# Kernel optimization log

Hardware: AMD Instinct MI355X
Metric: run time of the kernel (lower is better)

Reference implementation:

```python
import jax, jax.numpy as jnp
import numpy as np

KP_EXTENT = 1.2  # influence radius of each kernel point (init arg KP_extent)
SHADOW_COORD = 1e6  # shadow point coordinate for padding (as in original KPConv)


def setup_inputs() -> dict:
    key = jax.random.key(0)
    k1, k2, k3, k4, k5, k6 = jax.random.split(key, 6)
    N, Ns, H, K, Cin, Cout = 20000, 20000, 40, 15, 128, 128
    q_pts = jax.random.uniform(k1, (N, 3), dtype=jnp.float32)
    s_pts = jax.random.uniform(k2, (Ns, 3), dtype=jnp.float32)
    neighb_inds = jax.random.randint(k3, (N, H), 0, Ns, dtype=jnp.int32)
    x = jax.random.normal(k4, (Ns, Cin), dtype=jnp.float32)
    # kernel point positions inside the sphere (stand-in for load_kernels output)
    kernel_points = jax.random.normal(k5, (K, 3), dtype=jnp.float32) * 0.5
    kernel_points = kernel_points.at[0].set(0.0)  # fixed='center'
    weights = jax.random.normal(k6, (K, Cin, Cout), dtype=jnp.float32) * (1.0 / np.sqrt(Cin))
    return {"q_pts": q_pts, "s_pts": s_pts, "neighb_inds": neighb_inds,
            "x": x, "kernel_points": kernel_points, "weights": weights}


def reference(q_pts, s_pts, neighb_inds, x, kernel_points, weights):
    # Pad support points with a far-away shadow point and features with a zero row,
    # so out-of-range neighbor index Ns contributes nothing (original KPConv trick).
    s_pad = jnp.concatenate([s_pts, jnp.full((1, s_pts.shape[1]), SHADOW_COORD, s_pts.dtype)], axis=0)
    x_pad = jnp.concatenate([x, jnp.zeros((1, x.shape[1]), x.dtype)], axis=0)

    # Gather neighbor coords, center on query points: [N, H, 3]
    neighbors = s_pad[neighb_inds] - q_pts[:, None, :]

    # Squared distance to every kernel point: [N, H, K]
    diff = neighbors[:, :, None, :] - kernel_points[None, None, :, :]
    sq_dist = jnp.sum(diff * diff, axis=-1)

    # Linear influence weights, aggregation_mode='sum': [N, K, H]
    all_weights = jnp.clip(1.0 - jnp.sqrt(sq_dist) / KP_EXTENT, 0.0, None)
    all_weights = jnp.swapaxes(all_weights, 1, 2)

    # Gather neighbor features: [N, H, Cin]
    neighb_x = x_pad[neighb_inds]

    # Influence-weighted aggregation over neighbors: [N, K, Cin]
    weighted = jnp.einsum('nkh,nhc->nkc', all_weights, neighb_x)

    # Per-kernel-point linear maps, summed over kernel points: [N, Cout]
    out = jnp.einsum('nkc,kcd->nd', weighted, weights)
    return out
```

## Files before the change

kernel.cpp:

```cpp
#include <hip/hip_runtime.h>

#define KP   15
#define HN   40
#define CIN  128
#define COUT 128
#define KDIM (KP*CIN)
#define KP_EXT_INV (1.0f/1.2f)

typedef __bf16 bf16x8 __attribute__((ext_vector_type(8)));
typedef float  f32x4  __attribute__((ext_vector_type(4)));

__device__ inline void async_copy16(const void* g, void* lds) {
    __builtin_amdgcn_global_load_lds(
        (const __attribute__((address_space(1))) unsigned int*)g,
        (__attribute__((address_space(3))) unsigned int*)lds, 16, 0, 0);
}

__global__ __launch_bounds__(256)
void kpconv_prep(const float* __restrict__ x, const float* __restrict__ W,
                 __bf16* __restrict__ xb, __bf16* __restrict__ Wt,
                 int nx_elems, int nxB)
{
    __shared__ float sW[32][133];
    const int b = blockIdx.x;
    const int t = threadIdx.x;

    if (b < nxB) {
        const int e0 = (b*256 + t) * 8;
        if (e0 + 8 <= nx_elems) {
            const float4 f0 = *(const float4*)(x + e0);
            const float4 f1 = *(const float4*)(x + e0 + 4);
            bf16x8 v;
            v[0]=(__bf16)f0.x; v[1]=(__bf16)f0.y; v[2]=(__bf16)f0.z; v[3]=(__bf16)f0.w;
            v[4]=(__bf16)f1.x; v[5]=(__bf16)f1.y; v[6]=(__bf16)f1.z; v[7]=(__bf16)f1.w;
            *(bf16x8*)(xb + e0) = v;
        } else {
            for (int e = e0; e < nx_elems; ++e) xb[e] = (__bf16)x[e];
        }
    } else {
        const int kc0 = (b - nxB) * 32;
        #pragma unroll
        for (int i = 0; i < 4; ++i) {
            const int off = t*4 + i*1024;
            const int r = off >> 7, c = off & 127;
            const float4 f = *(const float4*)(W + (size_t)(kc0 + r)*COUT + c);
            sW[r][c+0]=f.x; sW[r][c+1]=f.y; sW[r][c+2]=f.z; sW[r][c+3]=f.w;
        }
        __syncthreads();
        #pragma unroll
        for (int i = 0; i < 2; ++i) {
            const int id = t + i*256;
            const int d  = id >> 2, ch = id & 3;
            bf16x8 v;
            #pragma unroll
            for (int j = 0; j < 8; ++j) v[j] = (__bf16)sW[ch*8 + j][d];
            *(bf16x8*)(Wt + (size_t)d*KDIM + kc0 + ch*8) = v;
        }
    }
}

__global__ __launch_bounds__(256, 4)
void kpconv_aggregate(const float* __restrict__ q_pts,
                      const float* __restrict__ s_pts,
                      const int*   __restrict__ nb,
                      const __bf16* __restrict__ xb,
                      const float* __restrict__ kpts,
                      __bf16* __restrict__ wsA,
                      int N, int Ns)
{
    __shared__ __align__(16) __bf16 sXt[4][4][128][8];
    __shared__ __align__(16) float4 s_nd[4][HN];
    __shared__ int                  s_idx[4][HN];

    const int t  = threadIdx.x;
    const int wv = t >> 6;
    const int l  = t & 63;
    const int n  = blockIdx.x * 4 + wv;

    if (l < HN) {
        int idx = nb[n*HN + l];
        float dx, dy, dz;
        if (idx >= 0 && idx < Ns) {
            dx = s_pts[idx*3+0] - q_pts[n*3+0];
            dy = s_pts[idx*3+1] - q_pts[n*3+1];
            dz = s_pts[idx*3+2] - q_pts[n*3+2];
        } else { idx = 0; dx = dy = dz = 2.0e6f; }
        s_idx[wv][l] = idx;
        s_nd[wv][l]  = make_float4(dx, dy, dz, 0.f);
    }
    __syncthreads();

    const int m = l & 15;
    const int q = l >> 4;
    float kx = 0.f, ky = 0.f, kz = 0.f;
    if (m < KP) { kx = kpts[m*3+0]; ky = kpts[m*3+1]; kz = kpts[m*3+2]; }

    bf16x8 wfrag[2];
    #pragma unroll
    for (int ks = 0; ks < 2; ++ks) {
        #pragma unroll
        for (int j = 0; j < 8; ++j) {
            const int h = ks*32 + q*8 + j;
            float w = 0.f;
            if (m < KP && h < HN) {
                float4 nd = s_nd[wv][h];
                float dx = nd.x - kx, dy = nd.y - ky, dz = nd.z - kz;
                w = fmaxf(1.0f - sqrtf(dx*dx + dy*dy + dz*dz) * KP_EXT_INV, 0.f);
            }
            wfrag[ks][j] = (__bf16)w;
        }
    }

    f32x4 acc[8];
    #pragma unroll
    for (int nt = 0; nt < 8; ++nt) acc[nt] = (f32x4){0.f, 0.f, 0.f, 0.f};

    const int c8 = l & 15;

    for (int ks = 0; ks < 2; ++ks) {
        const int hpBeg = ks ? 16 : 0;
        const int hpEnd = ks ? 20 : 16;
        for (int hp = hpBeg + (l >> 4); hp < hpEnd; hp += 4) {
            const int h0 = 2*hp;
            const uint4 a = *(const uint4*)(xb + (size_t)s_idx[wv][h0  ]*CIN + c8*8);
            const uint4 bb= *(const uint4*)(xb + (size_t)s_idx[wv][h0+1]*CIN + c8*8);
            const unsigned int av[4] = {a.x, a.y, a.z, a.w};
            const unsigned int bv[4] = {bb.x, bb.y, bb.z, bb.w};
            const int hl = h0 - ks*32;
            const int hc = hl >> 3;
            const int dw = hp & 3;
            unsigned int* plane = (unsigned int*)&sXt[wv][hc][0][0];
            #pragma unroll
            for (int j = 0; j < 8; ++j) {
                const unsigned int lo = (av[j>>1] >> ((j&1)*16)) & 0xFFFFu;
                const unsigned int hi = (bv[j>>1] >> ((j&1)*16)) & 0xFFFFu;
                const int p = c8*8 + (j ^ (c8 & 7));
                plane[p*4 + dw] = lo | (hi << 16);
            }
        }
        __syncthreads();

        #pragma unroll
        for (int nt = 0; nt < 8; ++nt) {
            const int cc = nt*16 + m;
            const int p  = (cc & ~7) | ((cc & 7) ^ ((cc >> 3) & 7));
            bf16x8 bfrag = *(const bf16x8*)&sXt[wv][q][p][0];
            acc[nt] = __builtin_amdgcn_mfma_f32_16x16x32_bf16(
                          wfrag[ks], bfrag, acc[nt], 0, 0, 0);
        }
        __syncthreads();
    }

    #pragma unroll
    for (int nt = 0; nt < 8; ++nt) {
        #pragma unroll
        for (int r = 0; r < 4; ++r) {
            const int row = q*4 + r;
            if (row < KP)
                wsA[(size_t)n*KDIM + row*CIN + nt*16 + m] = (__bf16)acc[nt][r];
        }
    }
}

#define BM 32
#define BK 128

__global__ __launch_bounds__(256, 2)
void kpconv_gemm(const __bf16* __restrict__ A,
                 const __bf16* __restrict__ Bt,
                 float* __restrict__ out, int M)
{
    __shared__ __align__(16) __bf16 sA[BM*BK];
    __shared__ __align__(16) __bf16 sB[COUT*BK];

    const int t     = threadIdx.x;
    const int wv    = t >> 6;
    const int l     = t & 63;
    const int mlane = l & 15;
    const int q     = l >> 4;
    const int m0    = blockIdx.x * BM;

    const int rA = t >> 4;
    const int pA = t & 15;

    f32x4 acc[2][2];
    #pragma unroll
    for (int i = 0; i < 2; ++i)
        #pragma unroll
        for (int j = 0; j < 2; ++j) acc[i][j] = (f32x4){0.f,0.f,0.f,0.f};

    for (int k0 = 0; k0 < KDIM; k0 += BK) {
        #pragma unroll
        for (int pass = 0; pass < 2; ++pass) {
            const int r  = rA + pass*16;
            const int ch = pA ^ (r & 15);
            async_copy16(A + (size_t)(m0 + r)*KDIM + k0 + ch*8,
                         (char*)sA + pass*4096 + wv*1024 + l*16);
        }
        #pragma unroll
        for (int pass = 0; pass < 8; ++pass) {
            const int r  = rA + pass*16;
            const int ch = pA ^ (r & 15);
            async_copy16(Bt + (size_t)r*KDIM + k0 + ch*8,
                         (char*)sB + pass*4096 + wv*1024 + l*16);
        }
        __syncthreads();

        #pragma unroll
        for (int ksi = 0; ksi < 4; ++ksi) {
            bf16x8 af[2], bfr[2];
            #pragma unroll
            for (int mt = 0; mt < 2; ++mt) {
                const int row = mt*16 + mlane;
                const int p   = (ksi*4 + q) ^ (row & 15);
                af[mt] = *(const bf16x8*)&sA[row*BK + p*8];
            }
            #pragma unroll
            for (int j = 0; j < 2; ++j) {
                const int row = (wv*2 + j)*16 + mlane;
                const int p   = (ksi*4 + q) ^ (row & 15);
                bfr[j] = *(const bf16x8*)&sB[row*BK + p*8];
            }
            #pragma unroll
            for (int mt = 0; mt < 2; ++mt)
                #pragma unroll
                for (int j = 0; j < 2; ++j)
                    acc[mt][j] = __builtin_amdgcn_mfma_f32_16x16x32_bf16(
                                     af[mt], bfr[j], acc[mt][j], 0, 0, 0);
        }
        __syncthreads();
    }

    #pragma unroll
    for (int mt = 0; mt < 2; ++mt)
        #pragma unroll
        for (int j = 0; j < 2; ++j)
            #pragma unroll
            for (int r = 0; r < 4; ++r)
                out[(size_t)(m0 + mt*16 + q*4 + r)*COUT + (wv*2+j)*16 + mlane]
                    = acc[mt][j][r];
}

#define TM 8
#define WSTR (KP*CIN + 4)

__global__ __launch_bounds__(256, 2)
void kpconv_fused(const float* __restrict__ q_pts,
                  const float* __restrict__ s_pts,
                  const int*   __restrict__ nb,
                  const float* __restrict__ x,
                  const float* __restrict__ kpts,
                  const float* __restrict__ W,
                  float* __restrict__ out,
                  int N, int Ns)
{
    __shared__ float s_kp[KP*3];
    __shared__ float s_nd2[HN*3];
    __shared__ int   s_idx2[HN];
    __shared__ float s_w[KP][HN];
    __shared__ float s_wt[TM*WSTR];

    const int t  = threadIdx.x;
    const int n0 = (int)blockIdx.x * TM;
    if (t < KP*3) s_kp[t] = kpts[t];
    const int c = t & (CIN-1);
    const int g = t >> 7;

    for (int m = 0; m < TM; ++m) {
        const int n = n0 + m;
        if (t < HN) {
            float dx = 1e6f, dy = 1e6f, dz = 1e6f;
            int idx = 0;
            if (n < N) {
                idx = nb[n*HN + t];
                if (idx >= 0 && idx < Ns) {
                    dx = s_pts[idx*3+0] - q_pts[n*3+0];
                    dy = s_pts[idx*3+1] - q_pts[n*3+1];
                    dz = s_pts[idx*3+2] - q_pts[n*3+2];
                } else idx = 0;
            }
            s_idx2[t] = idx;
            s_nd2[t*3+0] = dx; s_nd2[t*3+1] = dy; s_nd2[t*3+2] = dz;
        }
        __syncthreads();
        for (int task = t; task < KP*HN; task += 256) {
            const int k = task / HN;
            const int h = task - k*HN;
            const float dx = s_nd2[h*3+0] - s_kp[k*3+0];
            const float dy = s_nd2[h*3+1] - s_kp[k*3+1];
            const float dz = s_nd2[h*3+2] - s_kp[k*3+2];
            s_w[k][h] = fmaxf(1.0f - sqrtf(dx*dx+dy*dy+dz*dz)*KP_EXT_INV, 0.0f);
        }
        __syncthreads();
        float facc[8];
        #pragma unroll
        for (int j = 0; j < 8; ++j) facc[j] = 0.0f;
        #pragma unroll 8
        for (int h = 0; h < HN; ++h) {
            const float xv = x[s_idx2[h]*CIN + c];
            #pragma unroll
            for (int j = 0; j < 8; ++j) {
                const int k = g + 2*j;
                if (k < KP) facc[j] += s_w[k][h] * xv;
            }
        }
        #pragma unroll
        for (int j = 0; j < 8; ++j) {
            const int k = g + 2*j;
            if (k < KP) s_wt[m*WSTR + k*CIN + c] = facc[j];
        }
        __syncthreads();
    }

    const int m3 = t >> 5;
    const int d0 = (t & 31) * 4;
    const float* wm = &s_wt[m3*WSTR];
    float ax = 0.f, ay = 0.f, az = 0.f, aw = 0.f;
    #pragma unroll 4
    for (int kc = 0; kc < KP*CIN; ++kc) {
        const float  wvv = wm[kc];
        const float4 wr = *(const float4*)&W[kc*COUT + d0];
        ax += wvv * wr.x; ay += wvv * wr.y; az += wvv * wr.z; aw += wvv * wr.w;
    }
    const int n = n0 + m3;
    if (n < N) {
        float4 o; o.x = ax; o.y = ay; o.z = az; o.w = aw;
        *(float4*)&out[n*COUT + d0] = o;
    }
}

extern "C" void kernel_launch(void* const* d_in, const int* in_sizes, int n_in,
                              void* d_out, int out_size, void* d_ws, size_t ws_size,
                              hipStream_t stream) {
    const float* q_pts = (const float*)d_in[0];
    const float* s_pts = (const float*)d_in[1];
    const int*   nb    = (const int*)  d_in[2];
    const float* x     = (const float*)d_in[3];
    const float* kpts  = (const float*)d_in[4];
    const float* W     = (const float*)d_in[5];
    float* out = (float*)d_out;

    const int N  = in_sizes[0] / 3;
    const int Ns = in_sizes[1] / 3;
    const int nx = in_sizes[3];

    const size_t needA = (size_t)N * KDIM * sizeof(__bf16);
    const size_t needB = (size_t)COUT * KDIM * sizeof(__bf16);
    const size_t needX = (size_t)nx * sizeof(__bf16);

    if (ws_size >= needA + needB + needX && (N % 4) == 0 && (N % BM) == 0
        && (KDIM % 32) == 0) {
        __bf16* wsA = (__bf16*)d_ws;
        __bf16* wsB = (__bf16*)((char*)d_ws + needA);
        __bf16* wsX = (__bf16*)((char*)d_ws + needA + needB);

        const int nxB = (nx/8 + 255) / 256;
        const int nwB = KDIM / 32;
        hipLaunchKernelGGL(kpconv_prep, dim3(nxB + nwB), dim3(256), 0, stream,
                           x, W, wsX, wsB, nx, nxB);
        hipLaunchKernelGGL(kpconv_aggregate, dim3(N/4), dim3(256), 0, stream,
                           q_pts, s_pts, nb, wsX, kpts, wsA, N, Ns);
        hipLaunchKernelGGL(kpconv_gemm, dim3(N/BM), dim3(256), 0, stream,
                           wsA, wsB, out, N);
    } else {
        const int grid = (N + TM - 1) / TM;
        hipLaunchKernelGGL(kpconv_fused, dim3(grid), dim3(256), 0, stream,
                           q_pts, s_pts, nb, x, kpts, W, out, N, Ns);
    }
}
```

Baseline: 146.1 us.

## Fuse neighbor aggregation and weight GEMM into one kernel via LDS

Replaces the separate aggregate and GEMM kernels with a single kernel in which each 512-thread block aggregates 16 points into a swizzled LDS tile and then multiplies it against the bf16 weight matrix read directly from global memory with register double-buffering. This removes the round trip of the N x 1920 bf16 intermediate through global memory and one kernel launch. It also uses v_perm for packing and replaces block barriers with lgkmcnt waits inside each wave. In exchange, occupancy drops to one large block per CU with heavy LDS use, and every block re-reads the full weight matrix from cache.

```diff
diff --git a/kernel.cpp b/kernel.cpp
--- a/kernel.cpp
+++ b/kernel.cpp
@@ -6,15 +6,12 @@
 #define COUT 128
 #define KDIM (KP*CIN)
 #define KP_EXT_INV (1.0f/1.2f)
+#define MB   16
+#define NW   8
 
 typedef __bf16 bf16x8 __attribute__((ext_vector_type(8)));
+typedef __bf16 bf16x4 __attribute__((ext_vector_type(4)));
 typedef float  f32x4  __attribute__((ext_vector_type(4)));
-
-__device__ inline void async_copy16(const void* g, void* lds) {
-    __builtin_amdgcn_global_load_lds(
-        (const __attribute__((address_space(1))) unsigned int*)g,
-        (__attribute__((address_space(3))) unsigned int*)lds, 16, 0, 0);
-}
 
 __global__ __launch_bounds__(256)
 void kpconv_prep(const float* __restrict__ x, const float* __restrict__ W,
@@ -59,186 +56,153 @@
     }
 }
 
-__global__ __launch_bounds__(256, 4)
-void kpconv_aggregate(const float* __restrict__ q_pts,
-                      const float* __restrict__ s_pts,
-                      const int*   __restrict__ nb,
-                      const __bf16* __restrict__ xb,
-                      const float* __restrict__ kpts,
-                      __bf16* __restrict__ wsA,
-                      int N, int Ns)
+__global__ __launch_bounds__(512, 1)
+void kpconv_main(const float* __restrict__ q_pts,
+                 const float* __restrict__ s_pts,
+                 const int*   __restrict__ nb,
+                 const __bf16* __restrict__ xb,
+                 const float* __restrict__ kpts,
+                 const __bf16* __restrict__ Wt,
+                 float* __restrict__ out, int N, int Ns)
 {
-    __shared__ __align__(16) __bf16 sXt[4][4][128][8];
-    __shared__ __align__(16) float4 s_nd[4][HN];
-    __shared__ int                  s_idx[4][HN];
+    __shared__ __align__(16) __bf16 sWgt[MB][KDIM];
+    __shared__ __align__(16) __bf16 sXt[NW][4][128][8];
+    __shared__ __align__(16) float4 s_nd[NW][HN];
+    __shared__ int                  s_idx[NW][HN];
 
     const int t  = threadIdx.x;
     const int wv = t >> 6;
     const int l  = t & 63;
-    const int n  = blockIdx.x * 4 + wv;
-
-    if (l < HN) {
-        int idx = nb[n*HN + l];
-        float dx, dy, dz;
-        if (idx >= 0 && idx < Ns) {
-            dx = s_pts[idx*3+0] - q_pts[n*3+0];
-            dy = s_pts[idx*3+1] - q_pts[n*3+1];
-            dz = s_pts[idx*3+2] - q_pts[n*3+2];
-        } else { idx = 0; dx = dy = dz = 2.0e6f; }
-        s_idx[wv][l] = idx;
-        s_nd[wv][l]  = make_float4(dx, dy, dz, 0.f);
-    }
-    __syncthreads();
-
-    const int m = l & 15;
-    const int q = l >> 4;
+    const int m  = l & 15;
+    const int q  = l >> 4;
+
     float kx = 0.f, ky = 0.f, kz = 0.f;
     if (m < KP) { kx = kpts[m*3+0]; ky = kpts[m*3+1]; kz = kpts[m*3+2]; }
 
-    bf16x8 wfrag[2];
+    for (int pt = 0; pt < 2; ++pt) {
+        const int point = wv*2 + pt;
+        const int n = blockIdx.x*MB + point;
+
+        if (l < HN) {
+            int idx = nb[n*HN + l];
+            float dx, dy, dz;
+            if (idx >= 0 && idx < Ns) {
+                dx = s_pts[idx*3+0] - q_pts[n*3+0];
+                dy = s_pts[idx*3+1] - q_pts[n*3+1];
+                dz = s_pts[idx*3+2] - q_pts[n*3+2];
+            } else { idx = 0; dx = dy = dz = 2.0e6f; }
+            s_idx[wv][l] = idx;
+            s_nd[wv][l]  = make_float4(dx, dy, dz, 0.f);
+        }
+        __asm__ __volatile__("s_waitcnt lgkmcnt(0)" ::: "memory");
+
+        bf16x8 wfrag[2];
+        #pragma unroll
+        for (int ks = 0; ks < 2; ++ks) {
+            #pragma unroll
+            for (int j = 0; j < 8; ++j) {
+                const int h = ks*32 + q*8 + j;
+                float w = 0.f;
+                if (m < KP && h < HN) {
+                    float4 nd = s_nd[wv][h];
+                    float dx = nd.x - kx, dy = nd.y - ky, dz = nd.z - kz;
+                    w = fmaxf(1.0f - sqrtf(dx*dx + dy*dy + dz*dz)*KP_EXT_INV, 0.f);
+                }
+                wfrag[ks][j] = (__bf16)w;
+            }
+        }
+
+        f32x4 acc[8];
+        #pragma unroll
+        for (int nt = 0; nt < 8; ++nt) acc[nt] = (f32x4){0.f,0.f,0.f,0.f};
+
+        #pragma unroll
+        for (int ks = 0; ks < 2; ++ks) {
+            const int iters = ks ? 1 : 4;
+            #pragma unroll
+            for (int it = 0; it < iters; ++it) {
+                const int hp = ks*16 + it*4 + q;
+                const int h0 = 2*hp;
+                const uint4 a  = *(const uint4*)(xb + (size_t)s_idx[wv][h0  ]*CIN + m*8);
+                const uint4 bb = *(const uint4*)(xb + (size_t)s_idx[wv][h0+1]*CIN + m*8);
+                const unsigned av[4] = {a.x, a.y, a.z, a.w};
+                const unsigned bv[4] = {bb.x, bb.y, bb.z, bb.w};
+                const int hl = h0 - ks*32;
+                const int hc = hl >> 3;
+                const int dw = hp & 3;
+                unsigned* plane = (unsigned*)&sXt[wv][hc][0][0];
+                #pragma unroll
+                for (int j = 0; j < 8; ++j) {
+                    const unsigned v = __builtin_amdgcn_perm(
+                        bv[j>>1], av[j>>1], (j&1) ? 0x07060302u : 0x05040100u);
+                    const int p = m*8 + (j ^ (m & 7));
+                    plane[p*4 + dw] = v;
+                }
+            }
+            __asm__ __volatile__("s_waitcnt lgkmcnt(0)" ::: "memory");
+
+            #pragma unroll
+            for (int nt = 0; nt < 8; ++nt) {
+                const int cc = nt*16 + m;
+                const int p  = (cc & ~7) | ((cc & 7) ^ ((cc >> 3) & 7));
+                bf16x8 xf = *(const bf16x8*)&sXt[wv][q][p][0];
+                acc[nt] = __builtin_amdgcn_mfma_f32_16x16x32_bf16(
+                              xf, wfrag[ks], acc[nt], 0, 0, 0);
+            }
+        }
+
+        if (m < KP) {
+            const int kpt = m;
+            #pragma unroll
+            for (int nt = 0; nt < 8; ++nt) {
+                bf16x4 v;
+                #pragma unroll
+                for (int r = 0; r < 4; ++r) v[r] = (__bf16)acc[nt][r];
+                const int c16  = kpt*16 + nt*2 + (q>>1);
+                const int c16s = (c16 & ~7) | ((c16 ^ kpt ^ point) & 7);
+                *(bf16x4*)((char*)&sWgt[point][0] + c16s*16 + (q&1)*8) = v;
+            }
+        }
+    }
+
+    __syncthreads();
+
+    const int d = wv*16 + m;
+    const __bf16* Wrow = Wt + (size_t)d*KDIM;
+
+    f32x4 cacc[4];
     #pragma unroll
-    for (int ks = 0; ks < 2; ++ks) {
-        #pragma unroll
-        for (int j = 0; j < 8; ++j) {
-            const int h = ks*32 + q*8 + j;
-            float w = 0.f;
-            if (m < KP && h < HN) {
-                float4 nd = s_nd[wv][h];
-                float dx = nd.x - kx, dy = nd.y - ky, dz = nd.z - kz;
-                w = fmaxf(1.0f - sqrtf(dx*dx + dy*dy + dz*dz) * KP_EXT_INV, 0.f);
-            }
-            wfrag[ks][j] = (__bf16)w;
-        }
-    }
-
-    f32x4 acc[8];
+    for (int g = 0; g < 4; ++g) cacc[g] = (f32x4){0.f,0.f,0.f,0.f};
+
+    bf16x8 bcur[4], bnxt[4];
     #pragma unroll
-    for (int nt = 0; nt < 8; ++nt) acc[nt] = (f32x4){0.f, 0.f, 0.f, 0.f};
-
-    const int c8 = l & 15;
-
-    for (int ks = 0; ks < 2; ++ks) {
-        const int hpBeg = ks ? 16 : 0;
-        const int hpEnd = ks ? 20 : 16;
-        for (int hp = hpBeg + (l >> 4); hp < hpEnd; hp += 4) {
-            const int h0 = 2*hp;
-            const uint4 a = *(const uint4*)(xb + (size_t)s_idx[wv][h0  ]*CIN + c8*8);
-            const uint4 bb= *(const uint4*)(xb + (size_t)s_idx[wv][h0+1]*CIN + c8*8);
-            const unsigned int av[4] = {a.x, a.y, a.z, a.w};
-            const unsigned int bv[4] = {bb.x, bb.y, bb.z, bb.w};
-            const int hl = h0 - ks*32;
-            const int hc = hl >> 3;
-            const int dw = hp & 3;
-            unsigned int* plane = (unsigned int*)&sXt[wv][hc][0][0];
-            #pragma unroll
-            for (int j = 0; j < 8; ++j) {
-                const unsigned int lo = (av[j>>1] >> ((j&1)*16)) & 0xFFFFu;
-                const unsigned int hi = (bv[j>>1] >> ((j&1)*16)) & 0xFFFFu;
-                const int p = c8*8 + (j ^ (c8 & 7));
-                plane[p*4 + dw] = lo | (hi << 16);
-            }
-        }
-        __syncthreads();
-
-        #pragma unroll
-        for (int nt = 0; nt < 8; ++nt) {
-            const int cc = nt*16 + m;
-            const int p  = (cc & ~7) | ((cc & 7) ^ ((cc >> 3) & 7));
-            bf16x8 bfrag = *(const bf16x8*)&sXt[wv][q][p][0];
-            acc[nt] = __builtin_amdgcn_mfma_f32_16x16x32_bf16(
-                          wfrag[ks], bfrag, acc[nt], 0, 0, 0);
-        }
-        __syncthreads();
-    }
-
+    for (int g = 0; g < 4; ++g)
+        bnxt[g] = *(const bf16x8*)(Wrow + g*32 + q*8);
+
+    for (int it = 0; it < 15; ++it) {
+        #pragma unroll
+        for (int g = 0; g < 4; ++g) bcur[g] = bnxt[g];
+        if (it < 14) {
+            #pragma unroll
+            for (int g = 0; g < 4; ++g)
+                bnxt[g] = *(const bf16x8*)(Wrow + (it+1)*128 + g*32 + q*8);
+        }
+        #pragma unroll
+        for (int g = 0; g < 4; ++g) {
+            const int c16  = it*16 + g*4 + q;
+            const int c16s = (c16 & ~7) | ((c16 ^ it ^ m) & 7);
+            bf16x8 af = *(const bf16x8*)((const char*)&sWgt[m][0] + c16s*16);
+            cacc[g] = __builtin_amdgcn_mfma_f32_16x16x32_bf16(
+                          af, bcur[g], cacc[g], 0, 0, 0);
+        }
+    }
+
+    cacc[0] += cacc[1]; cacc[2] += cacc[3]; cacc[0] += cacc[2];
+
+    const int p0 = blockIdx.x*MB + q*4;
     #pragma unroll
-    for (int nt = 0; nt < 8; ++nt) {
-        #pragma unroll
-        for (int r = 0; r < 4; ++r) {
-            const int row = q*4 + r;
-            if (row < KP)
-                wsA[(size_t)n*KDIM + row*CIN + nt*16 + m] = (__bf16)acc[nt][r];
-        }
-    }
-}
-
-#define BM 32
-#define BK 128
-
-__global__ __launch_bounds__(256, 2)
-void kpconv_gemm(const __bf16* __restrict__ A,
-                 const __bf16* __restrict__ Bt,
-                 float* __restrict__ out, int M)
-{
-    __shared__ __align__(16) __bf16 sA[BM*BK];
-    __shared__ __align__(16) __bf16 sB[COUT*BK];
-
-    const int t     = threadIdx.x;
-    const int wv    = t >> 6;
-    const int l     = t & 63;
-    const int mlane = l & 15;
-    const int q     = l >> 4;
-    const int m0    = blockIdx.x * BM;
-
-    const int rA = t >> 4;
-    const int pA = t & 15;
-
-    f32x4 acc[2][2];
-    #pragma unroll
-    for (int i = 0; i < 2; ++i)
-        #pragma unroll
-        for (int j = 0; j < 2; ++j) acc[i][j] = (f32x4){0.f,0.f,0.f,0.f};
-
-    for (int k0 = 0; k0 < KDIM; k0 += BK) {
-        #pragma unroll
-        for (int pass = 0; pass < 2; ++pass) {
-            const int r  = rA + pass*16;
-            const int ch = pA ^ (r & 15);
-            async_copy16(A + (size_t)(m0 + r)*KDIM + k0 + ch*8,
-                         (char*)sA + pass*4096 + wv*1024 + l*16);
-        }
-        #pragma unroll
-        for (int pass = 0; pass < 8; ++pass) {
-            const int r  = rA + pass*16;
-            const int ch = pA ^ (r & 15);
-            async_copy16(Bt + (size_t)r*KDIM + k0 + ch*8,
-                         (char*)sB + pass*4096 + wv*1024 + l*16);
-        }
-        __syncthreads();
-
-        #pragma unroll
-        for (int ksi = 0; ksi < 4; ++ksi) {
-            bf16x8 af[2], bfr[2];
-            #pragma unroll
-            for (int mt = 0; mt < 2; ++mt) {
-                const int row = mt*16 + mlane;
-                const int p   = (ksi*4 + q) ^ (row & 15);
-                af[mt] = *(const bf16x8*)&sA[row*BK + p*8];
-            }
-            #pragma unroll
-            for (int j = 0; j < 2; ++j) {
-                const int row = (wv*2 + j)*16 + mlane;
-                const int p   = (ksi*4 + q) ^ (row & 15);
-                bfr[j] = *(const bf16x8*)&sB[row*BK + p*8];
-            }
-            #pragma unroll
-            for (int mt = 0; mt < 2; ++mt)
-                #pragma unroll
-                for (int j = 0; j < 2; ++j)
-                    acc[mt][j] = __builtin_amdgcn_mfma_f32_16x16x32_bf16(
-                                     af[mt], bfr[j], acc[mt][j], 0, 0, 0);
-        }
-        __syncthreads();
-    }
-
-    #pragma unroll
-    for (int mt = 0; mt < 2; ++mt)
-        #pragma unroll
-        for (int j = 0; j < 2; ++j)
-            #pragma unroll
-            for (int r = 0; r < 4; ++r)
-                out[(size_t)(m0 + mt*16 + q*4 + r)*COUT + (wv*2+j)*16 + mlane]
-                    = acc[mt][j][r];
+    for (int r = 0; r < 4; ++r)
+        out[(size_t)(p0 + r)*COUT + wv*16 + m] = cacc[0][r];
 }
 
 #define TM 8
@@ -266,8 +230,8 @@
     const int c = t & (CIN-1);
     const int g = t >> 7;
 
-    for (int m = 0; m < TM; ++m) {
-        const int n = n0 + m;
+    for (int mm = 0; mm < TM; ++mm) {
+        const int n = n0 + mm;
         if (t < HN) {
             float dx = 1e6f, dy = 1e6f, dz = 1e6f;
             int idx = 0;
@@ -307,7 +271,7 @@
         #pragma unroll
         for (int j = 0; j < 8; ++j) {
             const int k = g + 2*j;
-            if (k < KP) s_wt[m*WSTR + k*CIN + c] = facc[j];
+            if (k < KP) s_wt[mm*WSTR + k*CIN + c] = facc[j];
         }
         __syncthreads();
     }
@@ -344,24 +308,19 @@
     const int Ns = in_sizes[1] / 3;
     const int nx = in_sizes[3];
 
-    const size_t needA = (size_t)N * KDIM * sizeof(__bf16);
     const size_t needB = (size_t)COUT * KDIM * sizeof(__bf16);
     const size_t needX = (size_t)nx * sizeof(__bf16);
 
-    if (ws_size >= needA + needB + needX && (N % 4) == 0 && (N % BM) == 0
-        && (KDIM % 32) == 0) {
-        __bf16* wsA = (__bf16*)d_ws;
-        __bf16* wsB = (__bf16*)((char*)d_ws + needA);
-        __bf16* wsX = (__bf16*)((char*)d_ws + needA + needB);
+    if (ws_size >= needB + needX && (N % MB) == 0 && (KDIM % 128) == 0) {
+        __bf16* wsB = (__bf16*)d_ws;
+        __bf16* wsX = (__bf16*)((char*)d_ws + needB);
 
         const int nxB = (nx/8 + 255) / 256;
         const int nwB = KDIM / 32;
         hipLaunchKernelGGL(kpconv_prep, dim3(nxB + nwB), dim3(256), 0, stream,
                            x, W, wsX, wsB, nx, nxB);
-        hipLaunchKernelGGL(kpconv_aggregate, dim3(N/4), dim3(256), 0, stream,
-                           q_pts, s_pts, nb, wsX, kpts, wsA, N, Ns);
-        hipLaunchKernelGGL(kpconv_gemm, dim3(N/BM), dim3(256), 0, stream,
-                           wsA, wsB, out, N);
+        hipLaunchKernelGGL(kpconv_main, dim3(N/MB), dim3(512), 0, stream,
+                           q_pts, s_pts, nb, wsX, kpts, wsB, out, N, Ns);
     } else {
         const int grid = (N + TM - 1) / TM;
         hipLaunchKernelGGL(kpconv_fused, dim3(grid), dim3(256), 0, stream,
```

Result: slower. 190.6 us (+30.4%).
